# Kernel tuning notes

Hardware: AMD Instinct MI355X
Metric: run time of the kernel (lower is better)

The kernel has to match this reference:

```python
import jax, jax.numpy as jnp
import numpy as np

FEATURE_DIM, HIDDEN_DIM, ATTN_DIM = 2048, 1024, 1024
B, L = 128, 196


def setup_inputs() -> dict:
    key = jax.random.key(0)
    ks = jax.random.split(key, 8)
    s_enc = 1.0 / np.sqrt(FEATURE_DIM)
    s_hid = 1.0 / np.sqrt(HIDDEN_DIM)
    s_full = 1.0 / np.sqrt(ATTN_DIM)
    return {
        "encoder_out": jax.random.normal(ks[0], (B, L, FEATURE_DIM), jnp.float32),
        "hidden": jax.random.normal(ks[1], (B, HIDDEN_DIM), jnp.float32),
        "W_enc": jax.random.uniform(ks[2], (FEATURE_DIM, ATTN_DIM), jnp.float32, -s_enc, s_enc),
        "b_enc": jax.random.uniform(ks[3], (ATTN_DIM,), jnp.float32, -s_enc, s_enc),
        "W_hid": jax.random.uniform(ks[4], (HIDDEN_DIM, ATTN_DIM), jnp.float32, -s_hid, s_hid),
        "b_hid": jax.random.uniform(ks[5], (ATTN_DIM,), jnp.float32, -s_hid, s_hid),
        "W_full": jax.random.uniform(ks[6], (ATTN_DIM,), jnp.float32, -s_full, s_full),
        "b_full": jax.random.uniform(ks[7], (1,), jnp.float32, -s_full, s_full),
    }


def reference(encoder_out, hidden, W_enc, b_enc, W_hid, b_hid, W_full, b_full):
    # attn1: (B, L, A)
    attn1 = jnp.einsum("blf,fa->bla", encoder_out, W_enc) + b_enc
    # attn2: (B, 1, A)
    attn2 = (hidden @ W_hid + b_hid)[:, None, :]
    attn = jax.nn.relu(attn1 + attn2)
    # scalar score per location: (B, L)
    scores = jnp.einsum("bla,a->bl", attn, W_full) + b_full[0]
    alpha = jax.nn.softmax(scores, axis=1)
    # weighted sum over L: (B, F)
    context = jnp.einsum("blf,bl->bf", encoder_out, alpha)
    return context, alpha
```

## Files before the change

kernel.cpp:

```cpp
#include <hip/hip_runtime.h>
#include <hip/hip_bf16.h>

typedef unsigned short u16;
typedef short s16x8 __attribute__((ext_vector_type(8)));
typedef unsigned int u32x2 __attribute__((ext_vector_type(2)));
typedef float f32x4 __attribute__((ext_vector_type(4)));

#define F_DIM 2048
#define A_DIM 1024
#define H_DIM 1024
#define BATCH 128
#define LLEN  196
#define MROWS (BATCH * LLEN)
#define MTILES (MROWS / 256)

__device__ __forceinline__ u16 f2b(float x) {
  union { float f; unsigned int u; } c; c.f = x;
  unsigned int r = (c.u + 0x7fffu + ((c.u >> 16) & 1u)) >> 16;
  return (u16)r;
}

__device__ __forceinline__ unsigned int f2b_pk(float a, float b) {
  unsigned int r;
  asm volatile("v_cvt_pk_bf16_f32 %0, %1, %2" : "=v"(r) : "v"(a), "v"(b));
  return r;
}

__device__ __forceinline__ void gload_lds16(const void* g, void* l) {
  __builtin_amdgcn_global_load_lds((const __attribute__((address_space(1))) void*)g,
                                   (__attribute__((address_space(3))) void*)l, 16, 0, 0);
}

__global__ void wenc_cvt_kernel(const float* __restrict__ W, u16* __restrict__ WT) {
  __shared__ float tile[32][33];
  int kb = blockIdx.x * 32, ab = blockIdx.y * 32;
  int t = threadIdx.x;
  int r = t >> 3, c = (t & 7) * 4;
  float4 v = *(const float4*)&W[(size_t)(kb + r) * A_DIM + ab + c];
  tile[r][c] = v.x; tile[r][c + 1] = v.y; tile[r][c + 2] = v.z; tile[r][c + 3] = v.w;
  __syncthreads();
  ushort4 o;
  o.x = f2b(tile[c + 0][r]);
  o.y = f2b(tile[c + 1][r]);
  o.z = f2b(tile[c + 2][r]);
  o.w = f2b(tile[c + 3][r]);
  *(ushort4*)&WT[(size_t)(ab + r) * F_DIM + kb + c] = o;
}

__global__ __launch_bounds__(256) void attn2_kernel(
    const float* __restrict__ hidden, const float* __restrict__ W_hid,
    const float* __restrict__ b_hid, const float* __restrict__ b_enc,
    float* __restrict__ attn2p) {
  __shared__ float hl[4][H_DIM];
  int t = threadIdx.x;
  int a  = blockIdx.x * 256 + t;
  int b0 = blockIdx.y * 4;
  float* hf = &hl[0][0];
  #pragma unroll
  for (int j = 0; j < 4; ++j) {
    int s = j * 256 + t;
    *(float4*)&hf[s * 4] = *(const float4*)&hidden[(size_t)b0 * H_DIM + s * 4];
  }
  __syncthreads();
  float acc[4] = {0.f, 0.f, 0.f, 0.f};
  #pragma unroll 4
  for (int k = 0; k < H_DIM; ++k) {
    float w = W_hid[(size_t)k * A_DIM + a];
    #pragma unroll
    for (int j = 0; j < 4; ++j) acc[j] = fmaf(hl[j][k], w, acc[j]);
  }
  float bias = b_hid[a] + b_enc[a];
  #pragma unroll
  for (int j = 0; j < 4; ++j)
    attn2p[(size_t)(b0 + j) * A_DIM + a] = acc[j] + bias;
}

__global__ __launch_bounds__(512, 2) void gemm_score(
    const float* __restrict__ enc, const u16* __restrict__ WT,
    const float* __restrict__ attn2p, const float* __restrict__ W_full,
    float* __restrict__ scores) {
  __shared__ __align__(16) u16 As[2 * 16384];
  __shared__ __align__(16) u16 Bs[2 * 16384];

  int i = blockIdx.x;
  int g = i >> 5, r = i & 31;
  int y = r >> 3, gi = r & 7;
  int mt = g * 8 + gi;
  if (mt >= MTILES) return;
  int m0 = mt * 256, n0 = y * 256;
  int t = threadIdx.x;
  int lane = t & 63, wave = t >> 6;
  int wr = wave >> 2, wc = wave & 3;
  int c16 = lane & 15, quad = lane >> 4;

  const float* aP = enc + (size_t)(m0 + (t >> 2)) * F_DIM + (t & 3) * 4;
  int awo[4];
  #pragma unroll
  for (int s = 0; s < 4; ++s)
    awo[s] = (t >> 2) * 64 + ((t & 3) & 1) * 4
           + (((s * 2 + ((t & 3) >> 1)) ^ ((t >> 2) & 7)) * 8);
  const u16* bgp = WT + (size_t)(n0 + (t >> 3)) * F_DIM + ((t & 7) ^ ((t >> 3) & 7)) * 8;

  const int akey = c16 & 7;
  int gsw[2];
  gsw[0] = ((0 * 4 + quad) ^ akey) * 8;
  gsw[1] = ((1 * 4 + quad) ^ akey) * 8;
  const int aro = (wr * 128 + c16) * 64;
  const int bro = (wc * 64 + c16) * 64;

  f32x4 acc[8][4];
  #pragma unroll
  for (int mi = 0; mi < 8; ++mi)
    #pragma unroll
    for (int ni = 0; ni < 4; ++ni) acc[mi][ni] = (f32x4){0.f, 0.f, 0.f, 0.f};

  s16x8 af[4][2], bf[2][2];
  float4 R0lo[4], R0hi[4], R1lo[4], R1hi[4];

#define ALD(RX, half, kt_) do {                                                 \
    const float* p_ = aP + (size_t)(half) * 128 * F_DIM + (kt_) * 64;           \
    RX[0] = *(const float4*)(p_);                                               \
    RX[1] = *(const float4*)(p_ + 16);                                          \
    RX[2] = *(const float4*)(p_ + 32);                                          \
    RX[3] = *(const float4*)(p_ + 48);                                          \
  } while (0)

#define AWR(RX, cb, half) do {                                                  \
    _Pragma("unroll")                                                           \
    for (int s_ = 0; s_ < 4; ++s_) {                                            \
      u32x2 w_; w_.x = f2b_pk(RX[s_].x, RX[s_].y);                              \
      w_.y = f2b_pk(RX[s_].z, RX[s_].w);                                        \
      *(u32x2*)&As[(cb) * 16384 + (half) * 8192 + awo[s_]] = w_;                \
    }                                                                           \
  } while (0)

#define BGL(cb, kt_) do {                                                       \
    _Pragma("unroll")                                                           \
    for (int s_ = 0; s_ < 4; ++s_)                                              \
      gload_lds16(bgp + (size_t)s_ * 64 * F_DIM + (size_t)(kt_) * 64,           \
                  Bs + (cb) * 16384 + s_ * 4096 + wave * 512);                  \
  } while (0)

#define DSRA(cb, mh)                                                            \
    _Pragma("unroll")                                                           \
    for (int i_ = 0; i_ < 4; ++i_)                                              \
      _Pragma("unroll")                                                         \
      for (int h_ = 0; h_ < 2; ++h_)                                            \
        af[i_][h_] = *(const s16x8*)&As[(cb) * 16384 + aro                      \
                                        + ((mh) * 4 + i_) * 1024 + gsw[h_]];

#define DSRB(cb, nh)                                                            \
    _Pragma("unroll")                                                           \
    for (int j_ = 0; j_ < 2; ++j_)                                              \
      _Pragma("unroll")                                                         \
      for (int h_ = 0; h_ < 2; ++h_)                                            \
        bf[j_][h_] = *(const s16x8*)&Bs[(cb) * 16384 + bro                      \
                                        + ((nh) * 2 + j_) * 1024 + gsw[h_]];

#define PHTAIL(mh, nh) do {                                                     \
    __builtin_amdgcn_s_barrier();                                               \
    asm volatile("s_waitcnt lgkmcnt(0)" ::: "memory");                          \
    __builtin_amdgcn_s_setprio(1);                                              \
    _Pragma("unroll")                                                           \
    for (int i_ = 0; i_ < 4; ++i_)                                              \
      _Pragma("unroll")                                                         \
      for (int j_ = 0; j_ < 2; ++j_)                                            \
        _Pragma("unroll")                                                       \
        for (int h_ = 0; h_ < 2; ++h_)                                          \
          acc[(mh) * 4 + i_][(nh) * 2 + j_] =                                   \
              __builtin_amdgcn_mfma_f32_16x16x32_bf16(                          \
                  af[i_][h_], bf[j_][h_],                                       \
                  acc[(mh) * 4 + i_][(nh) * 2 + j_], 0, 0, 0);                  \
    __builtin_amdgcn_s_setprio(0);                                              \
    __builtin_amdgcn_s_barrier();                                               \
  } while (0)

#define GROUP(T_, RB_, WB_, WLO_, WHI_, LLO_, LHI_) do {                        \
    int kB_ = min((T_) + 1, 31);                                                \
    int kA_ = min((T_) + 2, 31);                                                \
                                                                        \
    DSRA(RB_, 0); DSRB(RB_, 0);                                                 \
    AWR(WLO_, WB_, 0);                                                          \
    BGL(WB_, kB_);                                                              \
    PHTAIL(0, 0);                                                               \
                                                                        \
    DSRB(RB_, 1);                                                               \
    AWR(WHI_, WB_, 1);                                                          \
    ALD(LLO_, 0, kA_);                                                          \
    PHTAIL(0, 1);                                                               \
                                                                        \
    DSRA(RB_, 1); DSRB(RB_, 0);                                                 \
    ALD(LHI_, 1, kA_);                                                          \
    PHTAIL(1, 0);                                                               \
                                                                        \
    DSRB(RB_, 1);                                                               \
    asm volatile("s_waitcnt vmcnt(8)" ::: "memory");                            \
    PHTAIL(1, 1);                                                               \
  } while (0)

  ALD(R0lo, 0, 0);
  ALD(R0hi, 1, 0);
  BGL(0, 0);
  asm volatile("s_waitcnt vmcnt(4)" ::: "memory");
  AWR(R0lo, 0, 0);
  AWR(R0hi, 0, 1);
  ALD(R1lo, 0, 1);
  ALD(R1hi, 1, 1);
  asm volatile("s_waitcnt vmcnt(8) lgkmcnt(0)" ::: "memory");
  __builtin_amdgcn_s_barrier();

  #pragma unroll 1
  for (int T = 0; T < 32; T += 2) {
    GROUP(T,     0, 1, R1lo, R1hi, R0lo, R0hi);
    GROUP(T + 1, 1, 0, R0lo, R0hi, R1lo, R1hi);
  }
#undef GROUP
#undef PHTAIL
#undef DSRA
#undef DSRB
#undef BGL
#undef AWR
#undef ALD

  int bfirst = m0 / LLEN;
  int bnd1 = (bfirst + 1) * LLEN, bnd2 = (bfirst + 2) * LLEN;
  int b1c = min(bfirst + 1, BATCH - 1), b2c = min(bfirst + 2, BATCH - 1);
  float wf[4], a2v0[4], a2v1[4], a2v2[4];
  #pragma unroll
  for (int ni = 0; ni < 4; ++ni) {
    int col = n0 + wc * 64 + ni * 16 + c16;
    wf[ni]   = W_full[col];
    a2v0[ni] = attn2p[(size_t)bfirst * A_DIM + col];
    a2v1[ni] = attn2p[(size_t)b1c * A_DIM + col];
    a2v2[ni] = attn2p[(size_t)b2c * A_DIM + col];
  }
  #pragma unroll
  for (int mi = 0; mi < 8; ++mi) {
    #pragma unroll
    for (int rr = 0; rr < 4; ++rr) {
      int row_g = m0 + wr * 128 + mi * 16 + quad * 4 + rr;
      float p = 0.f;
      #pragma unroll
      for (int ni = 0; ni < 4; ++ni) {
        float a2 = row_g >= bnd1 ? (row_g >= bnd2 ? a2v2[ni] : a2v1[ni]) : a2v0[ni];
        float v = acc[mi][ni][rr] + a2;
        v = fmaxf(v, 0.f);
        p = fmaf(v, wf[ni], p);
      }
      p += __shfl_xor(p, 1);
      p += __shfl_xor(p, 2);
      p += __shfl_xor(p, 4);
      p += __shfl_xor(p, 8);
      if (c16 == 0) atomicAdd(&scores[row_g], p);
    }
  }
}

__global__ void softmax_kernel(const float* __restrict__ scores, float* __restrict__ alpha) {
  __shared__ float red[8];
  int b = blockIdx.x, t = threadIdx.x;
  float s = (t < LLEN) ? scores[b * LLEN + t] : -3.0e38f;
  float m = s;
  #pragma unroll
  for (int o = 1; o <= 32; o <<= 1) m = fmaxf(m, __shfl_xor(m, o));
  if ((t & 63) == 0) red[t >> 6] = m;
  __syncthreads();
  m = fmaxf(fmaxf(red[0], red[1]), fmaxf(red[2], red[3]));
  float e = (t < LLEN) ? expf(s - m) : 0.f;
  float sum = e;
  #pragma unroll
  for (int o = 1; o <= 32; o <<= 1) sum += __shfl_xor(sum, o);
  __syncthreads();
  if ((t & 63) == 0) red[4 + (t >> 6)] = sum;
  __syncthreads();
  sum = red[4] + red[5] + red[6] + red[7];
  if (t < LLEN) alpha[b * LLEN + t] = e / sum;
}

__global__ __launch_bounds__(256) void context_kernel(
    const float* __restrict__ enc, const float* __restrict__ alpha,
    float* __restrict__ out) {
  __shared__ float al[LLEN];
  __shared__ float4 part[4][64];
  int b = blockIdx.y, t = threadIdx.x;
  if (t < LLEN) al[t] = alpha[b * LLEN + t];
  __syncthreads();
  int f4 = blockIdx.x * 64 + (t & 63);
  int lq = t >> 6;
  const float4* e4 = (const float4*)enc
                   + ((size_t)b * LLEN + lq * 49) * (F_DIM / 4) + f4;
  float4 acc = {0.f, 0.f, 0.f, 0.f};
  #pragma unroll 7
  for (int j = 0; j < 49; ++j) {
    float4 v = e4[(size_t)j * (F_DIM / 4)];
    float a = al[lq * 49 + j];
    acc.x = fmaf(v.x, a, acc.x);
    acc.y = fmaf(v.y, a, acc.y);
    acc.z = fmaf(v.z, a, acc.z);
    acc.w = fmaf(v.w, a, acc.w);
  }
  part[lq][t & 63] = acc;
  __syncthreads();
  if (t < 64) {
    float4 p0 = part[0][t], p1 = part[1][t], p2 = part[2][t], p3 = part[3][t];
    float4 s;
    s.x = (p0.x + p1.x) + (p2.x + p3.x);
    s.y = (p0.y + p1.y) + (p2.y + p3.y);
    s.z = (p0.z + p1.z) + (p2.z + p3.z);
    s.w = (p0.w + p1.w) + (p2.w + p3.w);
    *(float4*)(out + (size_t)b * F_DIM + (size_t)(blockIdx.x * 64 + t) * 4) = s;
  }
}

extern "C" void kernel_launch(void* const* d_in, const int* in_sizes, int n_in,
                              void* d_out, int out_size, void* d_ws, size_t ws_size,
                              hipStream_t stream) {
  const float* enc    = (const float*)d_in[0];
  const float* hidden = (const float*)d_in[1];
  const float* W_enc  = (const float*)d_in[2];
  const float* b_enc  = (const float*)d_in[3];
  const float* W_hid  = (const float*)d_in[4];
  const float* b_hid  = (const float*)d_in[5];
  const float* W_full = (const float*)d_in[6];
  float* out = (float*)d_out;
  float* alpha_out = out + (size_t)BATCH * F_DIM;

  const size_t wt_bytes = (size_t)A_DIM * F_DIM * sizeof(u16);
  const size_t a2_bytes = (size_t)BATCH * A_DIM * sizeof(float);
  const size_t sc_bytes = (size_t)MROWS * sizeof(float);
  char* ws = (char*)d_ws;
  u16*   WT     = (u16*)ws;
  float* attn2p = (float*)(ws + wt_bytes);
  float* scores = (float*)(ws + wt_bytes + a2_bytes);

  hipMemsetAsync(scores, 0, sc_bytes, stream);

  wenc_cvt_kernel<<<dim3(F_DIM / 32, A_DIM / 32), 256, 0, stream>>>(W_enc, WT);
  attn2_kernel<<<dim3(A_DIM / 256, BATCH / 4), 256, 0, stream>>>(hidden, W_hid, b_hid, b_enc, attn2p);
  gemm_score<<<dim3(416), 512, 0, stream>>>(enc, WT, attn2p, W_full, scores);
  softmax_kernel<<<dim3(BATCH), 256, 0, stream>>>(scores, alpha_out);
  context_kernel<<<dim3(8, BATCH), 256, 0, stream>>>(enc, alpha_out, out);
}
```

Baseline: 550.9 us.

## Split-K attn2 with atomics and reschedule GEMM phases with double-buffered B fragments

The attn2 projection now splits the hidden dimension across a third grid axis, handles 8 batch rows per block and accumulates partial results with atomicAdd into a zeroed buffer, which raises parallelism for this small GEMV-like kernel. In the main GEMM, B fragments are kept in two register sets so the B reload between phases can be dropped. Global A loads and B async loads are moved earlier, and the LDS writes of A are moved later, to overlap memory traffic with MFMA work. The costs are more registers in the occupancy-bound GEMM, atomic contention, and a summation order that is no longer deterministic.

```diff
diff --git a/kernel.cpp b/kernel.cpp
--- a/kernel.cpp
+++ b/kernel.cpp
@@ -47,32 +47,34 @@
   *(ushort4*)&WT[(size_t)(ab + r) * F_DIM + kb + c] = o;
 }
 
-__global__ __launch_bounds__(256) void attn2_kernel(
-    const float* __restrict__ hidden, const float* __restrict__ W_hid,
-    const float* __restrict__ b_hid, const float* __restrict__ b_enc,
-    float* __restrict__ attn2p) {
-  __shared__ float hl[4][H_DIM];
+__global__ void attn2_kernel(const float* __restrict__ hidden, const float* __restrict__ W_hid,
+                             const float* __restrict__ b_hid, const float* __restrict__ b_enc,
+                             float* __restrict__ attn2p) {
+  __shared__ float hl[8][128];
   int t = threadIdx.x;
   int a  = blockIdx.x * 256 + t;
-  int b0 = blockIdx.y * 4;
-  float* hf = &hl[0][0];
-  #pragma unroll
-  for (int j = 0; j < 4; ++j) {
-    int s = j * 256 + t;
-    *(float4*)&hf[s * 4] = *(const float4*)&hidden[(size_t)b0 * H_DIM + s * 4];
-  }
-  __syncthreads();
-  float acc[4] = {0.f, 0.f, 0.f, 0.f};
+  int b0 = blockIdx.y * 8;
+  int k0 = blockIdx.z * 128;
+  {
+    int j = t >> 5, kk = (t & 31) * 4;
+    float4 v = *(const float4*)&hidden[(size_t)(b0 + j) * H_DIM + k0 + kk];
+    hl[j][kk + 0] = v.x; hl[j][kk + 1] = v.y; hl[j][kk + 2] = v.z; hl[j][kk + 3] = v.w;
+  }
+  __syncthreads();
+  float acc[8] = {0.f, 0.f, 0.f, 0.f, 0.f, 0.f, 0.f, 0.f};
   #pragma unroll 4
-  for (int k = 0; k < H_DIM; ++k) {
-    float w = W_hid[(size_t)k * A_DIM + a];
+  for (int k = 0; k < 128; ++k) {
+    float w = W_hid[(size_t)(k0 + k) * A_DIM + a];
     #pragma unroll
-    for (int j = 0; j < 4; ++j) acc[j] = fmaf(hl[j][k], w, acc[j]);
-  }
-  float bias = b_hid[a] + b_enc[a];
-  #pragma unroll
-  for (int j = 0; j < 4; ++j)
-    attn2p[(size_t)(b0 + j) * A_DIM + a] = acc[j] + bias;
+    for (int j = 0; j < 8; ++j) acc[j] = fmaf(hl[j][k], w, acc[j]);
+  }
+  if (blockIdx.z == 0) {
+    float bias = b_hid[a] + b_enc[a];
+    #pragma unroll
+    for (int j = 0; j < 8; ++j) acc[j] += bias;
+  }
+  #pragma unroll
+  for (int j = 0; j < 8; ++j) atomicAdd(&attn2p[(size_t)(b0 + j) * A_DIM + a], acc[j]);
 }
 
 __global__ __launch_bounds__(512, 2) void gemm_score(
@@ -114,7 +116,7 @@
     #pragma unroll
     for (int ni = 0; ni < 4; ++ni) acc[mi][ni] = (f32x4){0.f, 0.f, 0.f, 0.f};
 
-  s16x8 af[4][2], bf[2][2];
+  s16x8 af[4][2], bf0[2][2], bf1[2][2];
   float4 R0lo[4], R0hi[4], R1lo[4], R1hi[4];
 
 #define ALD(RX, half, kt_) do {                                                 \
@@ -149,15 +151,15 @@
         af[i_][h_] = *(const s16x8*)&As[(cb) * 16384 + aro                      \
                                         + ((mh) * 4 + i_) * 1024 + gsw[h_]];
 
-#define DSRB(cb, nh)                                                            \
+#define DSRB(BF, cb, nh)                                                        \
     _Pragma("unroll")                                                           \
     for (int j_ = 0; j_ < 2; ++j_)                                              \
       _Pragma("unroll")                                                         \
       for (int h_ = 0; h_ < 2; ++h_)                                            \
-        bf[j_][h_] = *(const s16x8*)&Bs[(cb) * 16384 + bro                      \
+        BF[j_][h_] = *(const s16x8*)&Bs[(cb) * 16384 + bro                      \
                                         + ((nh) * 2 + j_) * 1024 + gsw[h_]];
 
-#define PHTAIL(mh, nh) do {                                                     \
+#define PHTAIL(BF, mh, nh) do {                                                 \
     __builtin_amdgcn_s_barrier();                                               \
     asm volatile("s_waitcnt lgkmcnt(0)" ::: "memory");                          \
     __builtin_amdgcn_s_setprio(1);                                              \
@@ -169,7 +171,7 @@
         for (int h_ = 0; h_ < 2; ++h_)                                          \
           acc[(mh) * 4 + i_][(nh) * 2 + j_] =                                   \
               __builtin_amdgcn_mfma_f32_16x16x32_bf16(                          \
-                  af[i_][h_], bf[j_][h_],                                       \
+                  af[i_][h_], BF[j_][h_],                                       \
                   acc[(mh) * 4 + i_][(nh) * 2 + j_], 0, 0, 0);                  \
     __builtin_amdgcn_s_setprio(0);                                              \
     __builtin_amdgcn_s_barrier();                                               \
@@ -179,23 +181,22 @@
     int kB_ = min((T_) + 1, 31);                                                \
     int kA_ = min((T_) + 2, 31);                                                \
                                                                         \
-    DSRA(RB_, 0); DSRB(RB_, 0);                                                 \
+    DSRA(RB_, 0); DSRB(bf0, RB_, 0);                                            \
+    BGL(WB_, kB_);                                                              \
+    ALD(LLO_, 0, kA_);                                                          \
+    PHTAIL(bf0, 0, 0);                                                          \
+                                                                        \
+    DSRB(bf1, RB_, 1);                                                          \
+    ALD(LHI_, 1, kA_);                                                          \
+    PHTAIL(bf1, 0, 1);                                                          \
+                                                                        \
+    DSRA(RB_, 1);                                                               \
     AWR(WLO_, WB_, 0);                                                          \
-    BGL(WB_, kB_);                                                              \
-    PHTAIL(0, 0);                                                               \
+    PHTAIL(bf0, 1, 0);                                                          \
                                                                         \
-    DSRB(RB_, 1);                                                               \
     AWR(WHI_, WB_, 1);                                                          \
-    ALD(LLO_, 0, kA_);                                                          \
-    PHTAIL(0, 1);                                                               \
-                                                                        \
-    DSRA(RB_, 1); DSRB(RB_, 0);                                                 \
-    ALD(LHI_, 1, kA_);                                                          \
-    PHTAIL(1, 0);                                                               \
-                                                                        \
-    DSRB(RB_, 1);                                                               \
     asm volatile("s_waitcnt vmcnt(8)" ::: "memory");                            \
-    PHTAIL(1, 1);                                                               \
+    PHTAIL(bf1, 1, 1);                                                          \
   } while (0)
 
   ALD(R0lo, 0, 0);
@@ -333,10 +334,10 @@
   float* attn2p = (float*)(ws + wt_bytes);
   float* scores = (float*)(ws + wt_bytes + a2_bytes);
 
-  hipMemsetAsync(scores, 0, sc_bytes, stream);
+  hipMemsetAsync(attn2p, 0, a2_bytes + sc_bytes, stream);
 
   wenc_cvt_kernel<<<dim3(F_DIM / 32, A_DIM / 32), 256, 0, stream>>>(W_enc, WT);
-  attn2_kernel<<<dim3(A_DIM / 256, BATCH / 4), 256, 0, stream>>>(hidden, W_hid, b_hid, b_enc, attn2p);
+  attn2_kernel<<<dim3(A_DIM / 256, BATCH / 8, H_DIM / 128), 256, 0, stream>>>(hidden, W_hid, b_hid, b_enc, attn2p);
   gemm_score<<<dim3(416), 512, 0, stream>>>(enc, WT, attn2p, W_full, scores);
   softmax_kernel<<<dim3(BATCH), 256, 0, stream>>>(scores, alpha_out);
   context_kernel<<<dim3(8, BATCH), 256, 0, stream>>>(enc, alpha_out, out);
```

Result: slower. 667.1 us (+21.1%).
